# Kernel tuning notes

Hardware: AMD Instinct MI355X
Metric: run time of the kernel (lower is better)

Reference implementation:

```python
import jax, jax.numpy as jnp
import numpy as np

IN_DIM, EDGE_DIM, HID = 128, 64, 128
N_A, N_B, E_AB, E_AA = 50000, 50000, 320000, 320000


def setup_inputs() -> dict:
    key = jax.random.key(0)
    ks = jax.random.split(key, 13)
    inv = lambda n: 1.0 / np.sqrt(n)
    return {
        "x_a": jax.random.normal(ks[0], (N_A, IN_DIM), jnp.float32),
        "x_b": jax.random.normal(ks[1], (N_B, IN_DIM), jnp.float32),
        "ei_ab": jax.random.randint(ks[2], (2, E_AB), 0, N_A),
        "ea_ab": jax.random.normal(ks[3], (E_AB, EDGE_DIM), jnp.float32),
        "ei_aa": jax.random.randint(ks[4], (2, E_AA), 0, N_A),
        "ea_aa": jax.random.normal(ks[5], (E_AA, EDGE_DIM), jnp.float32),
        "Wh_w": jax.random.normal(ks[6], (EDGE_DIM, HID), jnp.float32) * inv(EDGE_DIM),
        "Wh_b": jnp.zeros((HID,), jnp.float32),
        "Wn_w": jax.random.normal(ks[7], (2 * IN_DIM, HID), jnp.float32) * inv(2 * IN_DIM),
        "Wn_b": jnp.zeros((HID,), jnp.float32),
        "w_e": jax.random.normal(ks[8], (HID,), jnp.float32) * inv(HID),
        "ft_w": jax.random.normal(ks[9], (IN_DIM, IN_DIM), jnp.float32) * inv(IN_DIM),
        "ft_b": jnp.zeros((IN_DIM,), jnp.float32),
    }


def reference(x_a, x_b, ei_ab, ea_ab, ei_aa, ea_aa,
              Wh_w, Wh_b, Wn_w, Wn_b, w_e, ft_w, ft_b):
    def edge_alpha(x_src, x_dst, ei, ea):
        # gather src/dst feats -> linear + relu -> score -> softmax over all edges
        s, d = ei[0], ei[1]
        nf = jnp.concatenate([x_src[s], x_dst[d]], axis=1)          # [E, 2*in_dim]
        h = jax.nn.relu(ea @ Wh_w + Wh_b + nf @ Wn_w + Wn_b)         # [E, hid]
        return jax.nn.softmax(h @ w_e, axis=0)                       # [E]

    alpha_ab = edge_alpha(x_a, x_b, ei_ab, ea_ab)
    alpha_aa = edge_alpha(x_a, x_a, ei_aa, ea_aa)

    lf_a = jnp.zeros_like(x_a)
    lf_b = jnp.zeros_like(x_b)
    s_ab, d_ab = ei_ab[0], ei_ab[1]
    # cross-type edge: scatter into both endpoint node types
    lf_a = lf_a.at[s_ab].add(-alpha_ab[:, None] * x_b[d_ab])
    lf_b = lf_b.at[d_ab].add(-alpha_ab[:, None] * x_a[s_ab])
    s_aa, d_aa = ei_aa[0], ei_aa[1]
    # same-type edge: single scatter (src side only, per original)
    lf_a = lf_a.at[s_aa].add(-alpha_aa[:, None] * x_a[d_aa])

    out_a = x_a + lf_a
    out_a = out_a + (out_a @ ft_w + ft_b)
    out_b = x_b + lf_b
    out_b = out_b + (out_b @ ft_w + ft_b)
    return out_a, out_b, alpha_ab, alpha_aa
```

## Files before the change

### kernel.cpp

```cpp
#include <hip/hip_runtime.h>
#include <hip/hip_fp16.h>
#include <cstdint>
#include <cstddef>

#define N_A   50000
#define N_B   50000
#define E_AB  320000
#define E_AA  320000
#define IN_DIM 128
#define HID    128
#define ED     64

using bf16x8 = __attribute__((ext_vector_type(8))) short;
using f32x4  = __attribute__((ext_vector_type(4))) float;
typedef unsigned short ushort_t;
typedef unsigned int   uint_t;

__device__ inline ushort_t bf16r(float f) {
    uint_t u = __float_as_uint(f);
    u = (u + 0x7FFF + ((u >> 16) & 1)) >> 16;
    return (ushort_t)u;
}
__device__ inline float bf2f(ushort_t h) {
    return __uint_as_float(((uint_t)h) << 16);
}
__device__ inline ushort_t f16r(float f) { return __half_as_ushort(__float2half_rn(f)); }
__device__ inline float f16f(ushort_t u) { return __half2float(__ushort_as_half(u)); }
__device__ inline uint_t packh2(float a, float b) {
    return (uint_t)f16r(a) | ((uint_t)f16r(b) << 16);
}

__device__ inline void online_merge(float& m, float& l, float om, float ol) {
    const float nm = fmaxf(m, om);
    l = l * __expf(m - nm) + ol * __expf(om - nm);
    m = nm;
}

__global__ __launch_bounds__(64) void prep_w_all(
    const float* __restrict__ Wh, const float* __restrict__ W1,
    const float* __restrict__ W2, const float* __restrict__ FT,
    const float* __restrict__ we,
    ushort_t* __restrict__ BhWh, ushort_t* __restrict__ BlWh,
    ushort_t* __restrict__ BhW1, ushort_t* __restrict__ BlW1,
    ushort_t* __restrict__ BhW2, ushort_t* __restrict__ BlW2,
    ushort_t* __restrict__ BhFT, ushort_t* __restrict__ BlFT,
    float* __restrict__ wep)
{
    const int f = blockIdx.x;
    const int lane = threadIdx.x;
    if (f == 112) {
#pragma unroll
        for (int q = 0; q < 2; ++q) {
            const int idx = lane + q * 64;
            const int l15 = idx >> 3, ct = idx & 7;
            wep[idx] = we[ct * 16 + l15];
        }
        return;
    }
    const float* W; ushort_t *oh, *ol; int KT, fl;
    if (f < 16)      { W = Wh; oh = BhWh; ol = BlWh; KT = 2; fl = f; }
    else if (f < 48) { W = W1; oh = BhW1; ol = BlW1; KT = 4; fl = f - 16; }
    else if (f < 80) { W = W2; oh = BhW2; ol = BlW2; KT = 4; fl = f - 48; }
    else             { W = FT; oh = BhFT; ol = BlFT; KT = 4; fl = f - 80; }
    const int ct = fl / KT, kt = fl % KT;
    const int col = ct * 16 + (lane & 15);
    const int kb  = kt * 32 + (lane >> 4) * 8;
#pragma unroll
    for (int j = 0; j < 8; ++j) {
        const float v = W[(kb + j) * 128 + col];
        const ushort_t h = bf16r(v);
        oh[(size_t)(fl * 64 + lane) * 8 + j] = h;
        ol[(size_t)(fl * 64 + lane) * 8 + j] = bf16r(v - bf2f(h));
    }
}

__global__ __launch_bounds__(256) void proj_dual_mfma(
    const float* __restrict__ X,
    const ushort_t* __restrict__ B1h, const ushort_t* __restrict__ B1l,
    const ushort_t* __restrict__ B2h, const ushort_t* __restrict__ B2l,
    const float* __restrict__ bh, const float* __restrict__ bn,
    ushort_t* __restrict__ P1, ushort_t* __restrict__ P2,
    ushort_t* __restrict__ X16, int N)
{
    const int lane = threadIdx.x & 63;
    const int l15 = lane & 15, lg = lane >> 4;
    const int r0 = blockIdx.x * 64 + (threadIdx.x >> 6) * 16;
    const int arow = (r0 + l15 < N) ? (r0 + l15) : (N - 1);

    bf16x8 ahi[4], alo[4];
#pragma unroll
    for (int kt = 0; kt < 4; ++kt) {
        float v[8];
        *(float4*)(v + 0) = *(const float4*)&X[(size_t)arow * 128 + kt * 32 + lg * 8];
        *(float4*)(v + 4) = *(const float4*)&X[(size_t)arow * 128 + kt * 32 + lg * 8 + 4];
        uint4 xu;
        xu.x = packh2(v[0], v[1]); xu.y = packh2(v[2], v[3]);
        xu.z = packh2(v[4], v[5]); xu.w = packh2(v[6], v[7]);
        *(uint4*)&X16[(size_t)arow * 128 + kt * 32 + lg * 8] = xu;
#pragma unroll
        for (int j = 0; j < 8; ++j) {
            const ushort_t h = bf16r(v[j]);
            ahi[kt][j] = (short)h;
            alo[kt][j] = (short)bf16r(v[j] - bf2f(h));
        }
    }

    f32x4 acc1[8], acc2[8];
#pragma unroll
    for (int ct = 0; ct < 8; ++ct) {
        const float b = bh[ct * 16 + l15] + bn[ct * 16 + l15];
        acc1[ct] = (f32x4){b, b, b, b};
        acc2[ct] = (f32x4){0.f, 0.f, 0.f, 0.f};
    }

#pragma unroll
    for (int ct = 0; ct < 8; ++ct) {
#pragma unroll
        for (int kt = 0; kt < 4; ++kt) {
            const size_t fo = (size_t)((ct * 4 + kt) * 64 + lane) * 8;
            const bf16x8 b1h = *(const bf16x8*)&B1h[fo];
            const bf16x8 b1l = *(const bf16x8*)&B1l[fo];
            const bf16x8 b2h = *(const bf16x8*)&B2h[fo];
            const bf16x8 b2l = *(const bf16x8*)&B2l[fo];
            acc1[ct] = __builtin_amdgcn_mfma_f32_16x16x32_bf16(ahi[kt], b1h, acc1[ct], 0, 0, 0);
            acc1[ct] = __builtin_amdgcn_mfma_f32_16x16x32_bf16(alo[kt], b1h, acc1[ct], 0, 0, 0);
            acc1[ct] = __builtin_amdgcn_mfma_f32_16x16x32_bf16(ahi[kt], b1l, acc1[ct], 0, 0, 0);
            acc2[ct] = __builtin_amdgcn_mfma_f32_16x16x32_bf16(ahi[kt], b2h, acc2[ct], 0, 0, 0);
            acc2[ct] = __builtin_amdgcn_mfma_f32_16x16x32_bf16(alo[kt], b2h, acc2[ct], 0, 0, 0);
            acc2[ct] = __builtin_amdgcn_mfma_f32_16x16x32_bf16(ahi[kt], b2l, acc2[ct], 0, 0, 0);
        }
    }
#pragma unroll
    for (int i = 0; i < 4; ++i) {
        const int row = r0 + lg * 4 + i;
        if (row < N) {
            uint4 u1, u2;
            u1.x = packh2(acc1[0][i], acc1[1][i]); u1.y = packh2(acc1[2][i], acc1[3][i]);
            u1.z = packh2(acc1[4][i], acc1[5][i]); u1.w = packh2(acc1[6][i], acc1[7][i]);
            u2.x = packh2(acc2[0][i], acc2[1][i]); u2.y = packh2(acc2[2][i], acc2[3][i]);
            u2.z = packh2(acc2[4][i], acc2[5][i]); u2.w = packh2(acc2[6][i], acc2[7][i]);
            *(uint4*)&P1[(size_t)row * 128 + l15 * 8] = u1;
            *(uint4*)&P2[(size_t)row * 128 + l15 * 8] = u2;
        }
    }
}

__global__ __launch_bounds__(256) void proj_single_mfma(
    const float* __restrict__ X,
    const ushort_t* __restrict__ Bh, const ushort_t* __restrict__ Bl,
    ushort_t* __restrict__ P, ushort_t* __restrict__ X16, int N)
{
    const int lane = threadIdx.x & 63;
    const int l15 = lane & 15, lg = lane >> 4;
    const int r0 = blockIdx.x * 64 + (threadIdx.x >> 6) * 16;
    const int arow = (r0 + l15 < N) ? (r0 + l15) : (N - 1);

    bf16x8 ahi[4], alo[4];
#pragma unroll
    for (int kt = 0; kt < 4; ++kt) {
        float v[8];
        *(float4*)(v + 0) = *(const float4*)&X[(size_t)arow * 128 + kt * 32 + lg * 8];
        *(float4*)(v + 4) = *(const float4*)&X[(size_t)arow * 128 + kt * 32 + lg * 8 + 4];
        uint4 xu;
        xu.x = packh2(v[0], v[1]); xu.y = packh2(v[2], v[3]);
        xu.z = packh2(v[4], v[5]); xu.w = packh2(v[6], v[7]);
        *(uint4*)&X16[(size_t)arow * 128 + kt * 32 + lg * 8] = xu;
#pragma unroll
        for (int j = 0; j < 8; ++j) {
            const ushort_t h = bf16r(v[j]);
            ahi[kt][j] = (short)h;
            alo[kt][j] = (short)bf16r(v[j] - bf2f(h));
        }
    }

    f32x4 acc[8];
#pragma unroll
    for (int ct = 0; ct < 8; ++ct) acc[ct] = (f32x4){0.f, 0.f, 0.f, 0.f};

#pragma unroll
    for (int ct = 0; ct < 8; ++ct) {
#pragma unroll
        for (int kt = 0; kt < 4; ++kt) {
            const size_t fo = (size_t)((ct * 4 + kt) * 64 + lane) * 8;
            const bf16x8 bhf = *(const bf16x8*)&Bh[fo];
            const bf16x8 blf = *(const bf16x8*)&Bl[fo];
            acc[ct] = __builtin_amdgcn_mfma_f32_16x16x32_bf16(ahi[kt], bhf, acc[ct], 0, 0, 0);
            acc[ct] = __builtin_amdgcn_mfma_f32_16x16x32_bf16(alo[kt], bhf, acc[ct], 0, 0, 0);
            acc[ct] = __builtin_amdgcn_mfma_f32_16x16x32_bf16(ahi[kt], blf, acc[ct], 0, 0, 0);
        }
    }
#pragma unroll
    for (int i = 0; i < 4; ++i) {
        const int row = r0 + lg * 4 + i;
        if (row < N) {
            uint4 u;
            u.x = packh2(acc[0][i], acc[1][i]); u.y = packh2(acc[2][i], acc[3][i]);
            u.z = packh2(acc[4][i], acc[5][i]); u.w = packh2(acc[6][i], acc[7][i]);
            *(uint4*)&P[(size_t)row * 128 + l15 * 8] = u;
        }
    }
}

__global__ __launch_bounds__(256) void edge_score_k(
    const float* __restrict__ ea,
    const int*   __restrict__ ei,
    const ushort_t* __restrict__ P1h,
    const ushort_t* __restrict__ P2h,
    const ushort_t* __restrict__ Bhi,
    const ushort_t* __restrict__ Blo,
    const float* __restrict__ wep,
    float* __restrict__ score,
    int* __restrict__ cntS, int* __restrict__ cntD,
    int* __restrict__ rkS, int* __restrict__ rkD,
    float* __restrict__ pm, float* __restrict__ pl,
    int dual, int E)
{
    const int t    = threadIdx.x;
    const int lane = t & 63;
    const int l15  = lane & 15;
    const int lg   = lane >> 4;
    const int wv   = t >> 6;
    const int eb   = blockIdx.x * 128;

    if (t < 128) {
        const int e = eb + t;
        const int s = ei[e];
        rkS[e] = atomicAdd(&cntS[s], 1);
        if (dual) {
            const int d = ei[(size_t)E + e];
            rkD[e] = atomicAdd(&cntD[d], 1);
        }
    }

    const int e0 = eb + wv * 32;

    bf16x8 ahi[2][2], alo[2][2];
#pragma unroll
    for (int tl = 0; tl < 2; ++tl) {
        const float* arow = &ea[(size_t)(e0 + tl * 16 + l15) * 64 + lg * 8];
        float af[16];
        *(float4*)(af + 0)  = *(const float4*)(arow + 0);
        *(float4*)(af + 4)  = *(const float4*)(arow + 4);
        *(float4*)(af + 8)  = *(const float4*)(arow + 32);
        *(float4*)(af + 12) = *(const float4*)(arow + 36);
#pragma unroll
        for (int kt = 0; kt < 2; ++kt) {
#pragma unroll
            for (int j = 0; j < 8; ++j) {
                const float v = af[kt * 8 + j];
                const ushort_t h = bf16r(v);
                ahi[tl][kt][j] = (short)h;
                alo[tl][kt][j] = (short)bf16r(v - bf2f(h));
            }
        }
    }

    f32x4 acc[2][8];
#pragma unroll
    for (int tl = 0; tl < 2; ++tl)
#pragma unroll
        for (int ct = 0; ct < 8; ++ct) acc[tl][ct] = (f32x4){0.f, 0.f, 0.f, 0.f};

#pragma unroll
    for (int ct = 0; ct < 8; ++ct) {
        const bf16x8 bh0 = *(const bf16x8*)&Bhi[(size_t)(ct * 2 + 0) * 512 + lane * 8];
        const bf16x8 bl0 = *(const bf16x8*)&Blo[(size_t)(ct * 2 + 0) * 512 + lane * 8];
        const bf16x8 bh1 = *(const bf16x8*)&Bhi[(size_t)(ct * 2 + 1) * 512 + lane * 8];
        const bf16x8 bl1 = *(const bf16x8*)&Blo[(size_t)(ct * 2 + 1) * 512 + lane * 8];
#pragma unroll
        for (int tl = 0; tl < 2; ++tl) {
            acc[tl][ct] = __builtin_amdgcn_mfma_f32_16x16x32_bf16(ahi[tl][0], bh0, acc[tl][ct], 0, 0, 0);
            acc[tl][ct] = __builtin_amdgcn_mfma_f32_16x16x32_bf16(alo[tl][0], bh0, acc[tl][ct], 0, 0, 0);
            acc[tl][ct] = __builtin_amdgcn_mfma_f32_16x16x32_bf16(ahi[tl][0], bl0, acc[tl][ct], 0, 0, 0);
            acc[tl][ct] = __builtin_amdgcn_mfma_f32_16x16x32_bf16(ahi[tl][1], bh1, acc[tl][ct], 0, 0, 0);
            acc[tl][ct] = __builtin_amdgcn_mfma_f32_16x16x32_bf16(alo[tl][1], bh1, acc[tl][ct], 0, 0, 0);
            acc[tl][ct] = __builtin_amdgcn_mfma_f32_16x16x32_bf16(ahi[tl][1], bl1, acc[tl][ct], 0, 0, 0);
        }
    }

    float w8[8];
    *(float4*)(w8 + 0) = *(const float4*)&wep[l15 * 8];
    *(float4*)(w8 + 4) = *(const float4*)&wep[l15 * 8 + 4];

    float part[2][4];
#pragma unroll
    for (int tl = 0; tl < 2; ++tl) {
        int sidx[4], didx[4];
#pragma unroll
        for (int i = 0; i < 4; ++i) {
            const int e = e0 + tl * 16 + lg * 4 + i;
            sidx[i] = ei[e];
            didx[i] = ei[(size_t)E + e];
        }
        uint4 p1u[4], p2u[4];
#pragma unroll
        for (int i = 0; i < 4; ++i) {
            p1u[i] = *(const uint4*)&P1h[(size_t)sidx[i] * 128 + l15 * 8];
            p2u[i] = *(const uint4*)&P2h[(size_t)didx[i] * 128 + l15 * 8];
        }
#pragma unroll
        for (int i = 0; i < 4; ++i) {
            const uint_t* u1 = (const uint_t*)&p1u[i];
            const uint_t* u2 = (const uint_t*)&p2u[i];
            float p = 0.f;
#pragma unroll
            for (int q = 0; q < 4; ++q) {
                const float pa1 = f16f((ushort_t)(u1[q] & 0xFFFF));
                const float pb1 = f16f((ushort_t)(u1[q] >> 16));
                const float pa2 = f16f((ushort_t)(u2[q] & 0xFFFF));
                const float pb2 = f16f((ushort_t)(u2[q] >> 16));
                const float h0 = acc[tl][2 * q][i] + pa1 + pa2;
                const float h1 = acc[tl][2 * q + 1][i] + pb1 + pb2;
                p = fmaf(fmaxf(h0, 0.f), w8[2 * q], p);
                p = fmaf(fmaxf(h1, 0.f), w8[2 * q + 1], p);
            }
            part[tl][i] = p;
        }
#pragma unroll
        for (int m = 8; m >= 1; m >>= 1) {
#pragma unroll
            for (int i = 0; i < 4; ++i) part[tl][i] += __shfl_xor(part[tl][i], m, 64);
        }
        if (l15 == 0) {
#pragma unroll
            for (int i = 0; i < 4; ++i) score[e0 + tl * 16 + lg * 4 + i] = part[tl][i];
        }
    }

    float mw = part[0][0];
#pragma unroll
    for (int tl = 0; tl < 2; ++tl)
#pragma unroll
        for (int i = 0; i < 4; ++i) mw = fmaxf(mw, part[tl][i]);
    float lw = 0.f;
#pragma unroll
    for (int tl = 0; tl < 2; ++tl)
#pragma unroll
        for (int i = 0; i < 4; ++i) lw += __expf(part[tl][i] - mw);
#pragma unroll
    for (int off = 16; off <= 32; off <<= 1) {
        const float om = __shfl_xor(mw, off, 64);
        const float ol = __shfl_xor(lw, off, 64);
        online_merge(mw, lw, om, ol);
    }
    __shared__ float smm[4], sll[4];
    if (lane == 0) { smm[wv] = mw; sll[wv] = lw; }
    __syncthreads();
    if (t == 0) {
        float M = smm[0], L = sll[0];
        for (int i = 1; i < 4; ++i) online_merge(M, L, smm[i], sll[i]);
        pm[blockIdx.x] = M;
        pl[blockIdx.x] = L;
    }
}

__global__ __launch_bounds__(1024) void softmax_final_kernel(
    const float* __restrict__ pm, const float* __restrict__ pl,
    float* __restrict__ ML, int nPart)
{
    const int type = blockIdx.x;
    const float* mi = pm + type * nPart;
    const float* li = pl + type * nPart;
    float m = -1e30f, l = 0.f;
    for (int i = threadIdx.x; i < nPart; i += 1024) online_merge(m, l, mi[i], li[i]);
#pragma unroll
    for (int off = 1; off < 64; off <<= 1) {
        const float om = __shfl_xor(m, off, 64);
        const float ol = __shfl_xor(l, off, 64);
        online_merge(m, l, om, ol);
    }
    __shared__ float smm[16], sll[16];
    const int w = threadIdx.x >> 6, lane = threadIdx.x & 63;
    if (lane == 0) { smm[w] = m; sll[w] = l; }
    __syncthreads();
    if (threadIdx.x == 0) {
        float M = smm[0], L = sll[0];
        for (int i = 1; i < 16; ++i) online_merge(M, L, smm[i], sll[i]);
        ML[type * 2]     = M;
        ML[type * 2 + 1] = L;
    }
}

__global__ __launch_bounds__(1024) void csr_scan_kernel(
    const int* __restrict__ cntA, int* __restrict__ offA,
    const int* __restrict__ cntB, int* __restrict__ offB, int N)
{
    const int* cnt = (blockIdx.x == 0) ? cntA : cntB;
    int* off = (blockIdx.x == 0) ? offA : offB;

    __shared__ int warpsum[16];
    const int t = threadIdx.x, lane = t & 63, w = t >> 6;
    int carry = 0;

    for (int base = 0; base < N; base += 1024) {
        const int i = base + t;
        const int v = (i < N) ? cnt[i] : 0;
        int x = v;
#pragma unroll
        for (int d = 1; d < 64; d <<= 1) {
            const int y = __shfl_up(x, d, 64);
            if (lane >= d) x += y;
        }
        if (lane == 63) warpsum[w] = x;
        __syncthreads();
        if (w == 0 && lane < 16) {
            int s = warpsum[lane];
#pragma unroll
            for (int d = 1; d < 16; d <<= 1) {
                const int y = __shfl_up(s, d, 64);
                if (lane >= d) s += y;
            }
            warpsum[lane] = s;
        }
        __syncthreads();
        const int excl = (x - v) + ((w > 0) ? warpsum[w - 1] : 0) + carry;
        if (i < N) off[i] = excl;
        carry += warpsum[15];
        __syncthreads();
    }
    if (t == 0) off[N] = carry;
}

__global__ __launch_bounds__(256) void csr_fill_kernel(
    const int* __restrict__ ei_ab, const int* __restrict__ ei_aa,
    float* __restrict__ scAB, float* __restrict__ scAA,
    const float* __restrict__ ML,
    const int* __restrict__ offA, const int* __restrict__ offB,
    const int* __restrict__ rkAab, const int* __restrict__ rkBab,
    const int* __restrict__ rkAaa,
    int2* __restrict__ idxA, int2* __restrict__ idxB)
{
    const int i = blockIdx.x * 256 + threadIdx.x;
    const float Mab = ML[0], rLab = 1.0f / ML[1];
    const float Maa = ML[2], rLaa = 1.0f / ML[3];
    if (i < E_AB) {
        const float a = __expf(scAB[i] - Mab) * rLab;
        scAB[i] = a;
        const int s = ei_ab[i], d = ei_ab[E_AB + i];
        const int ab = __float_as_int(a);
        int pA = offA[s] + rkAab[i]; if (pA > 2 * E_AB - 1) pA = 2 * E_AB - 1;
        int pB = offB[d] + rkBab[i]; if (pB > E_AB - 1) pB = E_AB - 1;
        idxA[pA] = make_int2(d | (1 << 20), ab);
        idxB[pB] = make_int2(s, ab);
    }
    if (i < E_AA) {
        const float a = __expf(scAA[i] - Maa) * rLaa;
        scAA[i] = a;
        const int s = ei_aa[i];
        const int daa = ei_aa[E_AA + i];
        int pA = offA[s] + rkAaa[i]; if (pA > 2 * E_AB - 1) pA = 2 * E_AB - 1;
        idxA[pA] = make_int2(daa, __float_as_int(a));
    }
}

__global__ __launch_bounds__(256) void gather_final(
    const int*  __restrict__ off, const int2* __restrict__ idx,
    const ushort_t* __restrict__ xa16, const ushort_t* __restrict__ xb16,
    const float* __restrict__ xself,
    const ushort_t* __restrict__ Bh, const ushort_t* __restrict__ Bl,
    const float* __restrict__ fb,
    float* __restrict__ T, int N)
{
    const int lane = threadIdx.x & 63;
    const int l15  = lane & 15, lg = lane >> 4;
    const int wv   = threadIdx.x >> 6;
    const int r0   = blockIdx.x * 64 + wv * 16;

    for (int s = 0; s < 4; ++s) {
        const int row = r0 + s * 4 + lg;
        if (row < N) {
            const int beg = off[row], end = off[row + 1];
            float a8[8];
            *(float4*)(a8 + 0) = *(const float4*)&xself[(size_t)row * 128 + l15 * 8];
            *(float4*)(a8 + 4) = *(const float4*)&xself[(size_t)row * 128 + l15 * 8 + 4];
            int e = beg;
            for (; e + 1 < end; e += 2) {
                const int2 q0 = idx[e];
                const int2 q1 = idx[e + 1];
                const float al0 = __int_as_float(q0.y);
                const float al1 = __int_as_float(q1.y);
                const ushort_t* s0 = (q0.x & (1 << 20)) ? xb16 : xa16;
                const ushort_t* s1 = (q1.x & (1 << 20)) ? xb16 : xa16;
                const uint4 f0 = *(const uint4*)&s0[(size_t)(q0.x & 0xFFFFF) * 128 + l15 * 8];
                const uint4 f1 = *(const uint4*)&s1[(size_t)(q1.x & 0xFFFFF) * 128 + l15 * 8];
                const uint_t* u0 = (const uint_t*)&f0;
                const uint_t* u1 = (const uint_t*)&f1;
#pragma unroll
                for (int k = 0; k < 4; ++k) {
                    a8[2 * k]     = fmaf(-al0, f16f((ushort_t)(u0[k] & 0xFFFF)), a8[2 * k]);
                    a8[2 * k + 1] = fmaf(-al0, f16f((ushort_t)(u0[k] >> 16)),    a8[2 * k + 1]);
                    a8[2 * k]     = fmaf(-al1, f16f((ushort_t)(u1[k] & 0xFFFF)), a8[2 * k]);
                    a8[2 * k + 1] = fmaf(-al1, f16f((ushort_t)(u1[k] >> 16)),    a8[2 * k + 1]);
                }
            }
            if (e < end) {
                const int2 q0 = idx[e];
                const float al0 = __int_as_float(q0.y);
                const ushort_t* s0 = (q0.x & (1 << 20)) ? xb16 : xa16;
                const uint4 f0 = *(const uint4*)&s0[(size_t)(q0.x & 0xFFFFF) * 128 + l15 * 8];
                const uint_t* u0 = (const uint_t*)&f0;
#pragma unroll
                for (int k = 0; k < 4; ++k) {
                    a8[2 * k]     = fmaf(-al0, f16f((ushort_t)(u0[k] & 0xFFFF)), a8[2 * k]);
                    a8[2 * k + 1] = fmaf(-al0, f16f((ushort_t)(u0[k] >> 16)),    a8[2 * k + 1]);
                }
            }
            *(float4*)&T[(size_t)row * 128 + l15 * 8]     = *(float4*)(a8 + 0);
            *(float4*)&T[(size_t)row * 128 + l15 * 8 + 4] = *(float4*)(a8 + 4);
        }
    }
    __syncthreads();

    const int arow = (r0 + l15 < N) ? (r0 + l15) : (N - 1);
    bf16x8 ahi[4], alo[4];
#pragma unroll
    for (int kt = 0; kt < 4; ++kt) {
        float v[8];
        *(float4*)(v + 0) = *(const float4*)&T[(size_t)arow * 128 + kt * 32 + lg * 8];
        *(float4*)(v + 4) = *(const float4*)&T[(size_t)arow * 128 + kt * 32 + lg * 8 + 4];
#pragma unroll
        for (int j = 0; j < 8; ++j) {
            const ushort_t h = bf16r(v[j]);
            ahi[kt][j] = (short)h;
            alo[kt][j] = (short)bf16r(v[j] - bf2f(h));
        }
    }

    f32x4 acc[8];
#pragma unroll
    for (int ct = 0; ct < 8; ++ct) {
        const float b = fb[ct * 16 + l15];
#pragma unroll
        for (int i = 0; i < 4; ++i) {
            const int row = r0 + lg * 4 + i;
            const int rr = (row < N) ? row : (N - 1);
            acc[ct][i] = T[(size_t)rr * 128 + ct * 16 + l15] + b;
        }
    }

#pragma unroll
    for (int ct = 0; ct < 8; ++ct) {
#pragma unroll
        for (int kt = 0; kt < 4; ++kt) {
            const size_t fo = (size_t)((ct * 4 + kt) * 64 + lane) * 8;
            const bf16x8 bhf = *(const bf16x8*)&Bh[fo];
            const bf16x8 blf = *(const bf16x8*)&Bl[fo];
            acc[ct] = __builtin_amdgcn_mfma_f32_16x16x32_bf16(ahi[kt], bhf, acc[ct], 0, 0, 0);
            acc[ct] = __builtin_amdgcn_mfma_f32_16x16x32_bf16(alo[kt], bhf, acc[ct], 0, 0, 0);
            acc[ct] = __builtin_amdgcn_mfma_f32_16x16x32_bf16(ahi[kt], blf, acc[ct], 0, 0, 0);
        }
    }
#pragma unroll
    for (int ct = 0; ct < 8; ++ct) {
#pragma unroll
        for (int i = 0; i < 4; ++i) {
            const int row = r0 + lg * 4 + i;
            if (row < N) T[(size_t)row * 128 + ct * 16 + l15] = acc[ct][i];
        }
    }
}

extern "C" void kernel_launch(void* const* d_in, const int* in_sizes, int n_in,
                              void* d_out, int out_size, void* d_ws, size_t ws_size,
                              hipStream_t stream)
{
    const float* x_a   = (const float*)d_in[0];
    const float* x_b   = (const float*)d_in[1];
    const int*   ei_ab = (const int*)d_in[2];
    const float* ea_ab = (const float*)d_in[3];
    const int*   ei_aa = (const int*)d_in[4];
    const float* ea_aa = (const float*)d_in[5];
    const float* Wh_w  = (const float*)d_in[6];
    const float* Wh_b  = (const float*)d_in[7];
    const float* Wn_w  = (const float*)d_in[8];
    const float* Wn_b  = (const float*)d_in[9];
    const float* w_e   = (const float*)d_in[10];
    const float* ft_w  = (const float*)d_in[11];
    const float* ft_b  = (const float*)d_in[12];

    float* out = (float*)d_out;
    float* ws  = (float*)d_ws;

    ushort_t* P1h  = (ushort_t*)(ws);
    ushort_t* P2ah = (ushort_t*)(ws + 3200000);
    ushort_t* P2bh = (ushort_t*)(ws + 6400000);
    ushort_t* xa16 = (ushort_t*)(ws + 9600000);
    ushort_t* xb16 = (ushort_t*)(ws + 12800000);
    int* rkAab = (int*)(ws + 16000000);
    int* rkBab = (int*)(ws + 16320000);
    int* rkAaa = (int*)(ws + 16640000);
    int* cntA  = (int*)(ws + 16960000);
    int* cntB  = (int*)(ws + 17010000);
    int* offA  = (int*)(ws + 17060000);
    int* offB  = (int*)(ws + 17110004);
    float* pm  = ws + 17160008;
    float* pl  = ws + 17165008;
    float* ML  = ws + 17170008;
    float* wep = ws + 17170016;
    ushort_t* FR = (ushort_t*)(ws + 17170208);
    ushort_t* BhWh = FR;
    ushort_t* BlWh = FR + 8192;
    ushort_t* BhW1 = FR + 16384;
    ushort_t* BlW1 = FR + 32768;
    ushort_t* BhW2 = FR + 49152;
    ushort_t* BlW2 = FR + 65536;
    ushort_t* BhFT = FR + 81920;
    ushort_t* BlFT = FR + 98304;
    int2* idxA = (int2*)(ws + 17230000);
    int2* idxB = (int2*)(ws + 18510000);

    float* TA   = out;
    float* TB   = out + 6400000;
    float* alAB = out + 12800000;
    float* alAA = out + 13120000;

    hipMemsetAsync(cntA, 0, 100000 * sizeof(int), stream);
    prep_w_all<<<113, 64, 0, stream>>>(Wh_w, Wn_w, Wn_w + 128 * 128, ft_w, w_e,
                                       BhWh, BlWh, BhW1, BlW1, BhW2, BlW2, BhFT, BlFT, wep);

    proj_dual_mfma<<<(N_A + 63) / 64, 256, 0, stream>>>(x_a, BhW1, BlW1, BhW2, BlW2,
                                                        Wh_b, Wn_b, P1h, P2ah, xa16, N_A);
    proj_single_mfma<<<(N_B + 63) / 64, 256, 0, stream>>>(x_b, BhW2, BlW2, P2bh, xb16, N_B);

    edge_score_k<<<E_AB / 128, 256, 0, stream>>>(ea_ab, ei_ab, P1h, P2bh, BhWh, BlWh, wep,
                                                 alAB, cntA, cntB, rkAab, rkBab,
                                                 pm, pl, 1, E_AB);
    edge_score_k<<<E_AA / 128, 256, 0, stream>>>(ea_aa, ei_aa, P1h, P2ah, BhWh, BlWh, wep,
                                                 alAA, cntA, cntA, rkAaa, rkAaa,
                                                 pm + 2500, pl + 2500, 0, E_AA);

    softmax_final_kernel<<<2, 1024, 0, stream>>>(pm, pl, ML, 2500);

    csr_scan_kernel<<<2, 1024, 0, stream>>>(cntA, offA, cntB, offB, N_A);
    csr_fill_kernel<<<(E_AB + 255) / 256, 256, 0, stream>>>(ei_ab, ei_aa, alAB, alAA, ML,
                                                            offA, offB, rkAab, rkBab, rkAaa,
                                                            idxA, idxB);

    gather_final<<<(N_A + 63) / 64, 256, 0, stream>>>(offA, idxA, xa16, xb16, x_a,
                                                      BhFT, BlFT, ft_b, TA, N_A);
    gather_final<<<(N_B + 63) / 64, 256, 0, stream>>>(offB, idxB, xa16, xb16, x_b,
                                                      BhFT, BlFT, ft_b, TB, N_B);

    (void)in_sizes; (void)n_in; (void)out_size; (void)ws_size;
}
```

Baseline: 338.0 us.

## Merge edge-score launches, stage weight fragments in LDS, widen gather unroll

```diff
diff --git a/kernel.cpp b/kernel.cpp
--- a/kernel.cpp
+++ b/kernel.cpp
@@ -202,141 +202,143 @@
 }
 
 __global__ __launch_bounds__(256) void edge_score_k(
-    const float* __restrict__ ea,
-    const int*   __restrict__ ei,
+    const float* __restrict__ ea_ab, const float* __restrict__ ea_aa,
+    const int*   __restrict__ ei_ab, const int*   __restrict__ ei_aa,
     const ushort_t* __restrict__ P1h,
-    const ushort_t* __restrict__ P2h,
-    const ushort_t* __restrict__ Bhi,
-    const ushort_t* __restrict__ Blo,
+    const ushort_t* __restrict__ P2ah, const ushort_t* __restrict__ P2bh,
+    const ushort_t* __restrict__ Bhi,  const ushort_t* __restrict__ Blo,
     const float* __restrict__ wep,
-    float* __restrict__ score,
-    int* __restrict__ cntS, int* __restrict__ cntD,
-    int* __restrict__ rkS, int* __restrict__ rkD,
-    float* __restrict__ pm, float* __restrict__ pl,
-    int dual, int E)
+    float* __restrict__ scAB, float* __restrict__ scAA,
+    int* __restrict__ cntA, int* __restrict__ cntB,
+    int* __restrict__ rkAab, int* __restrict__ rkBab, int* __restrict__ rkAaa,
+    float* __restrict__ pm, float* __restrict__ pl)
 {
     const int t    = threadIdx.x;
     const int lane = t & 63;
     const int l15  = lane & 15;
     const int lg   = lane >> 4;
     const int wv   = t >> 6;
-    const int eb   = blockIdx.x * 128;
-
-    if (t < 128) {
+    const int type = (blockIdx.x >= 5000);
+    const int bb   = type ? (blockIdx.x - 5000) : blockIdx.x;
+    const int eb   = bb * 64;
+
+    const float* __restrict__ ea  = type ? ea_aa : ea_ab;
+    const int*   __restrict__ ei  = type ? ei_aa : ei_ab;
+    const ushort_t* __restrict__ P2h = type ? P2ah : P2bh;
+    float* __restrict__ score = type ? scAA : scAB;
+
+    __shared__ ushort_t sBh[8192];
+    __shared__ ushort_t sBl[8192];
+    {
+        const uint4* gh = (const uint4*)Bhi;
+        const uint4* gl = (const uint4*)Blo;
+        uint4* sh = (uint4*)sBh;
+        uint4* sl = (uint4*)sBl;
+#pragma unroll
+        for (int i = 0; i < 4; ++i) {
+            sh[t + i * 256] = gh[t + i * 256];
+            sl[t + i * 256] = gl[t + i * 256];
+        }
+    }
+
+    if (t < 64) {
         const int e = eb + t;
         const int s = ei[e];
-        rkS[e] = atomicAdd(&cntS[s], 1);
-        if (dual) {
-            const int d = ei[(size_t)E + e];
-            rkD[e] = atomicAdd(&cntD[d], 1);
-        }
-    }
-
-    const int e0 = eb + wv * 32;
-
-    bf16x8 ahi[2][2], alo[2][2];
-#pragma unroll
-    for (int tl = 0; tl < 2; ++tl) {
-        const float* arow = &ea[(size_t)(e0 + tl * 16 + l15) * 64 + lg * 8];
-        float af[16];
-        *(float4*)(af + 0)  = *(const float4*)(arow + 0);
-        *(float4*)(af + 4)  = *(const float4*)(arow + 4);
-        *(float4*)(af + 8)  = *(const float4*)(arow + 32);
-        *(float4*)(af + 12) = *(const float4*)(arow + 36);
-#pragma unroll
-        for (int kt = 0; kt < 2; ++kt) {
-#pragma unroll
-            for (int j = 0; j < 8; ++j) {
-                const float v = af[kt * 8 + j];
-                const ushort_t h = bf16r(v);
-                ahi[tl][kt][j] = (short)h;
-                alo[tl][kt][j] = (short)bf16r(v - bf2f(h));
-            }
-        }
-    }
-
-    f32x4 acc[2][8];
-#pragma unroll
-    for (int tl = 0; tl < 2; ++tl)
-#pragma unroll
-        for (int ct = 0; ct < 8; ++ct) acc[tl][ct] = (f32x4){0.f, 0.f, 0.f, 0.f};
+        const int r = atomicAdd(&cntA[s], 1);
+        if (type) rkAaa[e] = r; else rkAab[e] = r;
+    } else if (t < 128 && !type) {
+        const int e = eb + (t - 64);
+        const int d = ei[(size_t)E_AB + e];
+        rkBab[e] = atomicAdd(&cntB[d], 1);
+    }
+
+    const int e0 = eb + wv * 16;
+
+    int sidx[4], didx[4];
+#pragma unroll
+    for (int i = 0; i < 4; ++i) {
+        const int e = e0 + lg * 4 + i;
+        sidx[i] = ei[e];
+        didx[i] = ei[(size_t)E_AB + e];
+    }
+    uint4 p1u[4], p2u[4];
+#pragma unroll
+    for (int i = 0; i < 4; ++i) {
+        p1u[i] = *(const uint4*)&P1h[(size_t)sidx[i] * 128 + l15 * 8];
+        p2u[i] = *(const uint4*)&P2h[(size_t)didx[i] * 128 + l15 * 8];
+    }
+
+    const float* arow = &ea[(size_t)(e0 + l15) * 64 + lg * 8];
+    float af[16];
+    *(float4*)(af + 0)  = *(const float4*)(arow + 0);
+    *(float4*)(af + 4)  = *(const float4*)(arow + 4);
+    *(float4*)(af + 8)  = *(const float4*)(arow + 32);
+    *(float4*)(af + 12) = *(const float4*)(arow + 36);
+
+    bf16x8 ahi0, alo0, ahi1, alo1;
+#pragma unroll
+    for (int j = 0; j < 8; ++j) {
+        const ushort_t h0 = bf16r(af[j]);
+        ahi0[j] = (short)h0;
+        alo0[j] = (short)bf16r(af[j] - bf2f(h0));
+        const ushort_t h1 = bf16r(af[8 + j]);
+        ahi1[j] = (short)h1;
+        alo1[j] = (short)bf16r(af[8 + j] - bf2f(h1));
+    }
+
+    __syncthreads();
+
+    f32x4 acc[8];
+#pragma unroll
+    for (int ct = 0; ct < 8; ++ct) acc[ct] = (f32x4){0.f, 0.f, 0.f, 0.f};
 
 #pragma unroll
     for (int ct = 0; ct < 8; ++ct) {
-        const bf16x8 bh0 = *(const bf16x8*)&Bhi[(size_t)(ct * 2 + 0) * 512 + lane * 8];
-        const bf16x8 bl0 = *(const bf16x8*)&Blo[(size_t)(ct * 2 + 0) * 512 + lane * 8];
-        const bf16x8 bh1 = *(const bf16x8*)&Bhi[(size_t)(ct * 2 + 1) * 512 + lane * 8];
-        const bf16x8 bl1 = *(const bf16x8*)&Blo[(size_t)(ct * 2 + 1) * 512 + lane * 8];
-#pragma unroll
-        for (int tl = 0; tl < 2; ++tl) {
-            acc[tl][ct] = __builtin_amdgcn_mfma_f32_16x16x32_bf16(ahi[tl][0], bh0, acc[tl][ct], 0, 0, 0);
-            acc[tl][ct] = __builtin_amdgcn_mfma_f32_16x16x32_bf16(alo[tl][0], bh0, acc[tl][ct], 0, 0, 0);
-            acc[tl][ct] = __builtin_amdgcn_mfma_f32_16x16x32_bf16(ahi[tl][0], bl0, acc[tl][ct], 0, 0, 0);
-            acc[tl][ct] = __builtin_amdgcn_mfma_f32_16x16x32_bf16(ahi[tl][1], bh1, acc[tl][ct], 0, 0, 0);
-            acc[tl][ct] = __builtin_amdgcn_mfma_f32_16x16x32_bf16(alo[tl][1], bh1, acc[tl][ct], 0, 0, 0);
-            acc[tl][ct] = __builtin_amdgcn_mfma_f32_16x16x32_bf16(ahi[tl][1], bl1, acc[tl][ct], 0, 0, 0);
-        }
+        const bf16x8 bh0 = *(const bf16x8*)&sBh[(ct * 2 + 0) * 512 + lane * 8];
+        const bf16x8 bl0 = *(const bf16x8*)&sBl[(ct * 2 + 0) * 512 + lane * 8];
+        const bf16x8 bh1 = *(const bf16x8*)&sBh[(ct * 2 + 1) * 512 + lane * 8];
+        const bf16x8 bl1 = *(const bf16x8*)&sBl[(ct * 2 + 1) * 512 + lane * 8];
+        acc[ct] = __builtin_amdgcn_mfma_f32_16x16x32_bf16(ahi0, bh0, acc[ct], 0, 0, 0);
+        acc[ct] = __builtin_amdgcn_mfma_f32_16x16x32_bf16(alo0, bh0, acc[ct], 0, 0, 0);
+        acc[ct] = __builtin_amdgcn_mfma_f32_16x16x32_bf16(ahi0, bl0, acc[ct], 0, 0, 0);
+        acc[ct] = __builtin_amdgcn_mfma_f32_16x16x32_bf16(ahi1, bh1, acc[ct], 0, 0, 0);
+        acc[ct] = __builtin_amdgcn_mfma_f32_16x16x32_bf16(alo1, bh1, acc[ct], 0, 0, 0);
+        acc[ct] = __builtin_amdgcn_mfma_f32_16x16x32_bf16(ahi1, bl1, acc[ct], 0, 0, 0);
     }
 
     float w8[8];
     *(float4*)(w8 + 0) = *(const float4*)&wep[l15 * 8];
     *(float4*)(w8 + 4) = *(const float4*)&wep[l15 * 8 + 4];
 
-    float part[2][4];
-#pragma unroll
-    for (int tl = 0; tl < 2; ++tl) {
-        int sidx[4], didx[4];
-#pragma unroll
-        for (int i = 0; i < 4; ++i) {
-            const int e = e0 + tl * 16 + lg * 4 + i;
-            sidx[i] = ei[e];
-            didx[i] = ei[(size_t)E + e];
-        }
-        uint4 p1u[4], p2u[4];
-#pragma unroll
-        for (int i = 0; i < 4; ++i) {
-            p1u[i] = *(const uint4*)&P1h[(size_t)sidx[i] * 128 + l15 * 8];
-            p2u[i] = *(const uint4*)&P2h[(size_t)didx[i] * 128 + l15 * 8];
-        }
-#pragma unroll
-        for (int i = 0; i < 4; ++i) {
-            const uint_t* u1 = (const uint_t*)&p1u[i];
-            const uint_t* u2 = (const uint_t*)&p2u[i];
-            float p = 0.f;
-#pragma unroll
-            for (int q = 0; q < 4; ++q) {
-                const float pa1 = f16f((ushort_t)(u1[q] & 0xFFFF));
-                const float pb1 = f16f((ushort_t)(u1[q] >> 16));
-                const float pa2 = f16f((ushort_t)(u2[q] & 0xFFFF));
-                const float pb2 = f16f((ushort_t)(u2[q] >> 16));
-                const float h0 = acc[tl][2 * q][i] + pa1 + pa2;
-                const float h1 = acc[tl][2 * q + 1][i] + pb1 + pb2;
-                p = fmaf(fmaxf(h0, 0.f), w8[2 * q], p);
-                p = fmaf(fmaxf(h1, 0.f), w8[2 * q + 1], p);
-            }
-            part[tl][i] = p;
-        }
-#pragma unroll
-        for (int m = 8; m >= 1; m >>= 1) {
-#pragma unroll
-            for (int i = 0; i < 4; ++i) part[tl][i] += __shfl_xor(part[tl][i], m, 64);
-        }
-        if (l15 == 0) {
-#pragma unroll
-            for (int i = 0; i < 4; ++i) score[e0 + tl * 16 + lg * 4 + i] = part[tl][i];
-        }
-    }
-
-    float mw = part[0][0];
-#pragma unroll
-    for (int tl = 0; tl < 2; ++tl)
-#pragma unroll
-        for (int i = 0; i < 4; ++i) mw = fmaxf(mw, part[tl][i]);
-    float lw = 0.f;
-#pragma unroll
-    for (int tl = 0; tl < 2; ++tl)
-#pragma unroll
-        for (int i = 0; i < 4; ++i) lw += __expf(part[tl][i] - mw);
+    float part[4];
+#pragma unroll
+    for (int i = 0; i < 4; ++i) {
+        const __half2* h1 = (const __half2*)&p1u[i];
+        const __half2* h2 = (const __half2*)&p2u[i];
+        float p = 0.f;
+#pragma unroll
+        for (int q = 0; q < 4; ++q) {
+            const float2 pf = __half22float2(__hadd2(h1[q], h2[q]));
+            const float v0 = acc[2 * q][i] + pf.x;
+            const float v1 = acc[2 * q + 1][i] + pf.y;
+            p = fmaf(fmaxf(v0, 0.f), w8[2 * q], p);
+            p = fmaf(fmaxf(v1, 0.f), w8[2 * q + 1], p);
+        }
+        part[i] = p;
+    }
+#pragma unroll
+    for (int m = 8; m >= 1; m >>= 1) {
+#pragma unroll
+        for (int i = 0; i < 4; ++i) part[i] += __shfl_xor(part[i], m, 64);
+    }
+    if (l15 == 0) {
+#pragma unroll
+        for (int i = 0; i < 4; ++i) score[e0 + lg * 4 + i] = part[i];
+    }
+
+    float mw = fmaxf(fmaxf(part[0], part[1]), fmaxf(part[2], part[3]));
+    float lw = __expf(part[0] - mw) + __expf(part[1] - mw)
+             + __expf(part[2] - mw) + __expf(part[3] - mw);
 #pragma unroll
     for (int off = 16; off <= 32; off <<= 1) {
         const float om = __shfl_xor(mw, off, 64);
@@ -474,35 +476,39 @@
             *(float4*)(a8 + 0) = *(const float4*)&xself[(size_t)row * 128 + l15 * 8];
             *(float4*)(a8 + 4) = *(const float4*)&xself[(size_t)row * 128 + l15 * 8 + 4];
             int e = beg;
-            for (; e + 1 < end; e += 2) {
-                const int2 q0 = idx[e];
-                const int2 q1 = idx[e + 1];
-                const float al0 = __int_as_float(q0.y);
-                const float al1 = __int_as_float(q1.y);
-                const ushort_t* s0 = (q0.x & (1 << 20)) ? xb16 : xa16;
-                const ushort_t* s1 = (q1.x & (1 << 20)) ? xb16 : xa16;
-                const uint4 f0 = *(const uint4*)&s0[(size_t)(q0.x & 0xFFFFF) * 128 + l15 * 8];
-                const uint4 f1 = *(const uint4*)&s1[(size_t)(q1.x & 0xFFFFF) * 128 + l15 * 8];
-                const uint_t* u0 = (const uint_t*)&f0;
-                const uint_t* u1 = (const uint_t*)&f1;
+            for (; e + 3 < end; e += 4) {
+                int2 q[4];
+#pragma unroll
+                for (int k = 0; k < 4; ++k) q[k] = idx[e + k];
+                uint4 f[4];
 #pragma unroll
                 for (int k = 0; k < 4; ++k) {
-                    a8[2 * k]     = fmaf(-al0, f16f((ushort_t)(u0[k] & 0xFFFF)), a8[2 * k]);
-                    a8[2 * k + 1] = fmaf(-al0, f16f((ushort_t)(u0[k] >> 16)),    a8[2 * k + 1]);
-                    a8[2 * k]     = fmaf(-al1, f16f((ushort_t)(u1[k] & 0xFFFF)), a8[2 * k]);
-                    a8[2 * k + 1] = fmaf(-al1, f16f((ushort_t)(u1[k] >> 16)),    a8[2 * k + 1]);
+                    const ushort_t* sp = (q[k].x & (1 << 20)) ? xb16 : xa16;
+                    f[k] = *(const uint4*)&sp[(size_t)(q[k].x & 0xFFFFF) * 128 + l15 * 8];
+                }
+#pragma unroll
+                for (int k = 0; k < 4; ++k) {
+                    const float al = __int_as_float(q[k].y);
+                    const __half2* hp = (const __half2*)&f[k];
+#pragma unroll
+                    for (int j = 0; j < 4; ++j) {
+                        const float2 vf = __half22float2(hp[j]);
+                        a8[2 * j]     = fmaf(-al, vf.x, a8[2 * j]);
+                        a8[2 * j + 1] = fmaf(-al, vf.y, a8[2 * j + 1]);
+                    }
                 }
             }
-            if (e < end) {
+            for (; e < end; ++e) {
                 const int2 q0 = idx[e];
-                const float al0 = __int_as_float(q0.y);
-                const ushort_t* s0 = (q0.x & (1 << 20)) ? xb16 : xa16;
-                const uint4 f0 = *(const uint4*)&s0[(size_t)(q0.x & 0xFFFFF) * 128 + l15 * 8];
-                const uint_t* u0 = (const uint_t*)&f0;
-#pragma unroll
-                for (int k = 0; k < 4; ++k) {
-                    a8[2 * k]     = fmaf(-al0, f16f((ushort_t)(u0[k] & 0xFFFF)), a8[2 * k]);
-                    a8[2 * k + 1] = fmaf(-al0, f16f((ushort_t)(u0[k] >> 16)),    a8[2 * k + 1]);
+                const float al = __int_as_float(q0.y);
+                const ushort_t* sp = (q0.x & (1 << 20)) ? xb16 : xa16;
+                const uint4 f0 = *(const uint4*)&sp[(size_t)(q0.x & 0xFFFFF) * 128 + l15 * 8];
+                const __half2* hp = (const __half2*)&f0;
+#pragma unroll
+                for (int j = 0; j < 4; ++j) {
+                    const float2 vf = __half22float2(hp[j]);
+                    a8[2 * j]     = fmaf(-al, vf.x, a8[2 * j]);
+                    a8[2 * j + 1] = fmaf(-al, vf.y, a8[2 * j + 1]);
                 }
             }
             *(float4*)&T[(size_t)row * 128 + l15 * 8]     = *(float4*)(a8 + 0);
@@ -594,10 +600,10 @@
     int* offA  = (int*)(ws + 17060000);
     int* offB  = (int*)(ws + 17110004);
     float* pm  = ws + 17160008;
-    float* pl  = ws + 17165008;
-    float* ML  = ws + 17170008;
-    float* wep = ws + 17170016;
-    ushort_t* FR = (ushort_t*)(ws + 17170208);
+    float* pl  = ws + 17170008;
+    float* ML  = ws + 17180008;
+    float* wep = ws + 17180016;
+    ushort_t* FR = (ushort_t*)(ws + 17180208);
     ushort_t* BhWh = FR;
     ushort_t* BlWh = FR + 8192;
     ushort_t* BhW1 = FR + 16384;
@@ -606,8 +612,8 @@
     ushort_t* BlW2 = FR + 65536;
     ushort_t* BhFT = FR + 81920;
     ushort_t* BlFT = FR + 98304;
-    int2* idxA = (int2*)(ws + 17230000);
-    int2* idxB = (int2*)(ws + 18510000);
+    int2* idxA = (int2*)(ws + 17240000);
+    int2* idxB = (int2*)(ws + 18520000);
 
     float* TA   = out;
     float* TB   = out + 6400000;
@@ -622,14 +628,12 @@
                                                         Wh_b, Wn_b, P1h, P2ah, xa16, N_A);
     proj_single_mfma<<<(N_B + 63) / 64, 256, 0, stream>>>(x_b, BhW2, BlW2, P2bh, xb16, N_B);
 
-    edge_score_k<<<E_AB / 128, 256, 0, stream>>>(ea_ab, ei_ab, P1h, P2bh, BhWh, BlWh, wep,
-                                                 alAB, cntA, cntB, rkAab, rkBab,
-                                                 pm, pl, 1, E_AB);
-    edge_score_k<<<E_AA / 128, 256, 0, stream>>>(ea_aa, ei_aa, P1h, P2ah, BhWh, BlWh, wep,
-                                                 alAA, cntA, cntA, rkAaa, rkAaa,
-                                                 pm + 2500, pl + 2500, 0, E_AA);
-
-    softmax_final_kernel<<<2, 1024, 0, stream>>>(pm, pl, ML, 2500);
+    edge_score_k<<<10000, 256, 0, stream>>>(ea_ab, ea_aa, ei_ab, ei_aa,
+                                            P1h, P2ah, P2bh, BhWh, BlWh, wep,
+                                            alAB, alAA, cntA, cntB,
+                                            rkAab, rkBab, rkAaa, pm, pl);
+
+    softmax_final_kernel<<<2, 1024, 0, stream>>>(pm, pl, ML, 5000);
 
     csr_scan_kernel<<<2, 1024, 0, stream>>>(cntA, offA, cntB, offB, N_A);
     csr_fill_kernel<<<(E_AB + 255) / 256, 256, 0, stream>>>(ei_ab, ei_aa, alAB, alAA, ML,
```

After: 331.9 us. Within noise of the previous version (-1.8%).
